# Kernel optimization log

Hardware: AMD Instinct MI355X
Metric: run time of the kernel (lower is better)

Reference implementation:

```python
import jax, jax.numpy as jnp
import numpy as np

NG = 1024      # graphs
NPG = 128      # nodes per graph (forced by lin1 = Linear(128*hid, 128))
N = NG * NPG   # 131072 nodes
DEG = 16       # avg in-graph degree
E = N * DEG    # 2,097,152 edges
IN, H = 4, 64


def setup_inputs() -> dict:
    key = jax.random.key(0)
    ks = jax.random.split(key, 24)
    x = jax.random.normal(ks[0], (N, IN), jnp.float32)
    # edges constrained within each 128-node graph
    src = jax.random.randint(ks[1], (E,), 0, NPG)
    dst = jax.random.randint(ks[2], (E,), 0, NPG)
    off = jnp.repeat(jnp.arange(NG, dtype=jnp.int32) * NPG, NPG * DEG)
    edge_index = jnp.stack([src.astype(jnp.int32) + off, dst.astype(jnp.int32) + off])
    g = lambda k, shp, fan: jax.random.normal(k, shp, jnp.float32) / np.float32(np.sqrt(fan))
    return {
        "x": x, "edge_index": edge_index,
        # GATv2Conv(4->64)
        "Wl": g(ks[3], (IN, H), IN), "bl": jnp.zeros((H,), jnp.float32),
        "Wr": g(ks[4], (IN, H), IN), "br": jnp.zeros((H,), jnp.float32),
        "att_v2": g(ks[5], (H,), H), "b_v2": jnp.zeros((H,), jnp.float32),
        # GATConv #1 (64->64)
        "Wg1": g(ks[6], (H, H), H), "as1": g(ks[7], (H,), H),
        "ad1": g(ks[8], (H,), H), "bg1": jnp.zeros((H,), jnp.float32),
        # GATConv #2 (64->64)
        "Wg2": g(ks[9], (H, H), H), "as2": g(ks[10], (H,), H),
        "ad2": g(ks[11], (H,), H), "bg2": jnp.zeros((H,), jnp.float32),
        # LayerNorm(64)
        "ln_g": jnp.ones((H,), jnp.float32), "ln_b": jnp.zeros((H,), jnp.float32),
        # heads: Linear(128*64 -> 128), Linear(128 -> 1)
        "W1": g(ks[12], (NPG * H, 128), NPG * H), "b1": jnp.zeros((128,), jnp.float32),
        "W2": g(ks[13], (128, 1), 128), "b2": jnp.zeros((1,), jnp.float32),
    }


def _seg_softmax(logits, seg):
    # stable softmax over edges grouped by destination node
    m = jax.ops.segment_max(logits, seg, num_segments=N)
    ex = jnp.exp(logits - m[seg])
    s = jax.ops.segment_sum(ex, seg, num_segments=N)
    return ex / (s[seg] + 1e-16)


def _gatv2(x, src, dst, Wl, bl, Wr, br, att, bias):
    xl = x @ Wl + bl                       # source transform [N,H]
    xr = x @ Wr + br                       # target transform [N,H]
    e = jax.nn.leaky_relu(xl[src] + xr[dst], 0.2) @ att   # [E]
    a = _seg_softmax(e, dst)
    out = jax.ops.segment_sum(a[:, None] * xl[src], dst, num_segments=N)
    return out + bias


def _gat(x, src, dst, W, a_src, a_dst, bias):
    # GATConv default: add self-loops
    loop = jnp.arange(N, dtype=src.dtype)
    s2 = jnp.concatenate([src, loop]); d2 = jnp.concatenate([dst, loop])
    xw = x @ W                             # [N,H]
    al_s = xw @ a_src; al_d = xw @ a_dst   # per-node attention halves [N]
    e = jax.nn.leaky_relu(al_s[s2] + al_d[d2], 0.2)
    a = _seg_softmax(e, d2)
    out = jax.ops.segment_sum(a[:, None] * xw[s2], d2, num_segments=N)
    return out + bias


def _layernorm(x, g, b, eps=1e-5):
    mu = jnp.mean(x, -1, keepdims=True)
    var = jnp.mean(jnp.square(x - mu), -1, keepdims=True)
    return (x - mu) * jax.lax.rsqrt(var + eps) * g + b


def reference(x, edge_index, Wl, bl, Wr, br, att_v2, b_v2,
              Wg1, as1, ad1, bg1, Wg2, as2, ad2, bg2,
              ln_g, ln_b, W1, b1, W2, b2):
    src, dst = edge_index[0], edge_index[1]
    h = jax.nn.leaky_relu(_gatv2(x, src, dst, Wl, bl, Wr, br, att_v2, b_v2), 0.01)
    h = _layernorm(h, ln_g, ln_b)
    h = jax.nn.relu(_gat(h, src, dst, Wg1, as1, ad1, bg1))
    h = jax.nn.relu(_gat(h, src, dst, Wg2, as2, ad2, bg2))
    # linearize: batch is sorted with exactly NPG nodes per graph -> reshape
    h = h.reshape(NG, NPG * H)
    h = jax.nn.leaky_relu(h @ W1 + b1, 0.01)
    return jax.nn.sigmoid(h @ W2 + b2)     # [NG, 1]
```

## Files before the change

kernel.cpp:

```cpp
#include <hip/hip_runtime.h>
#include <hip/hip_bf16.h>

#define NGRAPH 1024
#define NPG 128
#define NTOT (NGRAPH*NPG)
#define EPG 2048
#define ETOT (NTOT*16)
#define HD 64

typedef unsigned int uint;
typedef unsigned short ushort_t;
typedef __attribute__((ext_vector_type(8))) short s8v;
typedef __attribute__((ext_vector_type(4))) float f32x4;

#define MFMA16 __builtin_amdgcn_mfma_f32_16x16x32_bf16

__device__ __forceinline__ float lrelu(float x, float s){ return fmaxf(x, x*s); }
__device__ __forceinline__ float b2lo(uint u){ return __uint_as_float(u << 16); }
__device__ __forceinline__ float b2hi(uint u){ return __uint_as_float(u & 0xFFFF0000u); }
__device__ __forceinline__ uint pkbf(float a, float b){
  union { __hip_bfloat162 h; uint u; } t;
  t.h = __hip_bfloat162{__float2bfloat16(a), __float2bfloat16(b)};
  return t.u;
}
__device__ __forceinline__ ushort_t bfb(float v){
  __hip_bfloat16 h = __float2bfloat16(v);
  union { __hip_bfloat16 h; ushort_t u; } t; t.h = h; return t.u;
}
union U4S8 { uint4 u; s8v s; };
__device__ __forceinline__ s8v bcs8(uint4 u){ U4S8 t; t.u = u; return t.s; }
__device__ __forceinline__ s8v pk8(uint4 x, uint4 y){
  U4S8 t;
  t.u.x = pkbf(__uint_as_float(x.x), __uint_as_float(x.y));
  t.u.y = pkbf(__uint_as_float(x.z), __uint_as_float(x.w));
  t.u.z = pkbf(__uint_as_float(y.x), __uint_as_float(y.y));
  t.u.w = pkbf(__uint_as_float(y.z), __uint_as_float(y.w));
  return t.s;
}

#define DPP_ADD(v, ctrl) ((v) + __int_as_float(__builtin_amdgcn_update_dpp(0, __float_as_int(v), (ctrl), 0xF, 0xF, false)))

__device__ __forceinline__ int oswz(int r, int p){ return (r<<5) | ((((p>>2) ^ (r & 7))<<2) | (p & 3)); }
__device__ __forceinline__ int obase(int r, int oc){ return (r<<5) | (((oc) ^ (r & 7))<<2); }
__device__ __forceinline__ int t64(int r, int p){ return (r<<6) | ((((p>>2) ^ (r & 15))<<2) | (p & 3)); }
__device__ __forceinline__ int t64b(int r, int q){ return (r<<6) | (((q ^ (r & 15))<<2)); }
__device__ __forceinline__ int fP(int r, int k){ return (r<<7) | (((((k>>2) ^ r) & 31)<<2) | (k & 3)); }
__device__ __forceinline__ int fPb(int r, int q){ return (r<<7) | ((((q ^ r) & 31))<<2); }

#define O_A   0
#define O_B   4096
#define O_P   8192
#define O_EV  10240
#define O_ED  11264
#define O_SOF 12288
#define O_SPO 12417
#define O_NMV 12545
#define O_SSE 12673
#define O_ALS 12801
#define O_ALD 12929
#define O_WAS 13060
#define O_WAD 13124
#define SM_SZ 13188

__global__ __launch_bounds__(256) void gnn_fused(
    const float* __restrict__ x, const int* __restrict__ ei,
    const float* __restrict__ Wl, const float* __restrict__ bl,
    const float* __restrict__ Wr, const float* __restrict__ br,
    const float* __restrict__ att, const float* __restrict__ bv2,
    const float* __restrict__ Wg1, const float* __restrict__ as1,
    const float* __restrict__ ad1, const float* __restrict__ bg1,
    const float* __restrict__ Wg2, const float* __restrict__ as2,
    const float* __restrict__ ad2, const float* __restrict__ bg2,
    const float* __restrict__ lng, const float* __restrict__ lnb,
    uint* __restrict__ hout)
{
  __shared__ uint SM[SM_SZ];
  uint*      sXl  = SM + O_A;
  uint*      sXr  = SM + O_B;
  float*     Pf   = (float*)(SM + O_P);
  _Float16*  evh  = (_Float16*)(SM + O_EV);
  ushort_t*  edsd = (ushort_t*)(SM + O_ED);
  int*       soff = (int*)(SM + O_SOF);
  int*       spos = (int*)(SM + O_SPO);
  float*     nmv  = (float*)(SM + O_NMV);
  float*     sse  = (float*)(SM + O_SSE);
  float*     als  = (float*)(SM + O_ALS);
  float*     ald  = (float*)(SM + O_ALD);
  float*     was  = (float*)(SM + O_WAS);
  float*     wad  = (float*)(SM + O_WAD);
  ushort_t*  sH16 = (ushort_t*)(SM + O_A);
  ushort_t*  sT16 = (ushort_t*)(SM + O_B);
  ushort_t*  wg16 = (ushort_t*)(SM + O_P);

  const int g    = blockIdx.x;
  const int tid  = threadIdx.x;
  const int lane = tid & 63;
  const int wv   = tid >> 6;
  const int lw   = lane & 15;
  const int lq   = lane >> 4;
  const int oc   = lane & 7;
  const int ebase = g * EPG;

  if (tid < NPG) spos[tid] = 0;
  __syncthreads();
  for (int e = tid; e < EPG; e += 256)
    atomicAdd(&spos[ei[ETOT + ebase + e] - g*NPG], 1);
  __syncthreads();
  if (wv == 0) {
    int c0 = spos[lane], c1 = spos[lane + 64];
    #pragma unroll
    for (int o = 1; o < 64; o <<= 1) { int t = __shfl_up(c0, o); if (lane >= o) c0 += t; }
    #pragma unroll
    for (int o = 1; o < 64; o <<= 1) { int t = __shfl_up(c1, o); if (lane >= o) c1 += t; }
    int tot0 = __shfl(c0, 63);
    soff[lane + 1]  = c0;
    soff[lane + 65] = c1 + tot0;
    if (lane == 0) soff[0] = 0;
  }
  __syncthreads();
  if (tid < NPG) spos[tid] = soff[tid];
  __syncthreads();
  for (int e = tid; e < EPG; e += 256) {
    int s = ei[ebase + e] - g*NPG;
    int d = ei[ETOT + ebase + e] - g*NPG;
    int p = atomicAdd(&spos[d], 1);
    edsd[p] = (ushort_t)(s | (d << 8));
  }

  {
    const int pl = lane & 31, hb = lane >> 5;
    const float2 wl0 = *(const float2*)&Wl[0*64 + 2*pl];
    const float2 wl1 = *(const float2*)&Wl[1*64 + 2*pl];
    const float2 wl2 = *(const float2*)&Wl[2*64 + 2*pl];
    const float2 wl3 = *(const float2*)&Wl[3*64 + 2*pl];
    const float2 wr0 = *(const float2*)&Wr[0*64 + 2*pl];
    const float2 wr1 = *(const float2*)&Wr[1*64 + 2*pl];
    const float2 wr2 = *(const float2*)&Wr[2*64 + 2*pl];
    const float2 wr3 = *(const float2*)&Wr[3*64 + 2*pl];
    const float2 blp = *(const float2*)&bl[2*pl];
    const float2 brp = *(const float2*)&br[2*pl];
    const float4* x4 = (const float4*)x + (size_t)g * NPG;
    __syncthreads();
    for (int st = 0; st < 16; st++) {
      int i = st*8 + wv*2 + hb;
      float4 xi = x4[i];
      float l0 = blp.x + xi.x*wl0.x + xi.y*wl1.x + xi.z*wl2.x + xi.w*wl3.x;
      float l1 = blp.y + xi.x*wl0.y + xi.y*wl1.y + xi.z*wl2.y + xi.w*wl3.y;
      float r0 = brp.x + xi.x*wr0.x + xi.y*wr1.x + xi.z*wr2.x + xi.w*wr3.x;
      float r1 = brp.y + xi.x*wr0.y + xi.y*wr1.y + xi.z*wr2.y + xi.w*wr3.y;
      sXl[oswz(i, pl)] = pkbf(l0, l1);
      sXr[oswz(i, pl)] = pkbf(r0, r1);
    }
  }
  __syncthreads();

  {
    const int grp = lane >> 3;
    float4 atA = *(const float4*)&att[oc*8];
    float4 atB = *(const float4*)&att[oc*8 + 4];
    int base = wv * 512;
    for (int stp = 0; stp < 64; stp++) {
      int e  = base + stp*8 + grp;
      int sd = edsd[e];
      int s  = sd & 127, d = sd >> 8;
      uint4 ql = *(uint4*)&sXl[obase(s, oc)];
      uint4 qr = *(uint4*)&sXr[obase(d, oc)];
      float acc, v;
      v = b2lo(ql.x)+b2lo(qr.x); acc  = lrelu(v,0.2f)*atA.x;
      v = b2hi(ql.x)+b2hi(qr.x); acc += lrelu(v,0.2f)*atA.y;
      v = b2lo(ql.y)+b2lo(qr.y); acc += lrelu(v,0.2f)*atA.z;
      v = b2hi(ql.y)+b2hi(qr.y); acc += lrelu(v,0.2f)*atA.w;
      v = b2lo(ql.z)+b2lo(qr.z); acc += lrelu(v,0.2f)*atB.x;
      v = b2hi(ql.z)+b2hi(qr.z); acc += lrelu(v,0.2f)*atB.y;
      v = b2lo(ql.w)+b2lo(qr.w); acc += lrelu(v,0.2f)*atB.z;
      v = b2hi(ql.w)+b2hi(qr.w); acc += lrelu(v,0.2f)*atB.w;
      acc = DPP_ADD(acc, 0x111); acc = DPP_ADD(acc, 0x112); acc = DPP_ADD(acc, 0x114);
      if ((lane & 7) == 7) Pf[e] = acc;
    }
  }
  __syncthreads();

  {
    const int g16 = tid >> 4, sl = tid & 15;
    for (int it = 0; it < 8; it++) {
      int d = it*16 + g16;
      int p0 = soff[d], p1 = soff[d+1];
      float m = -1e30f;
      for (int p = p0 + sl; p < p1; p += 16) m = fmaxf(m, Pf[p]);
      #pragma unroll
      for (int o = 1; o < 16; o <<= 1) m = fmaxf(m, __shfl_xor(m, o));
      float ssum = 0.f;
      for (int p = p0 + sl; p < p1; p += 16) {
        float ex = __expf(Pf[p] - m); ssum += ex; evh[p] = (_Float16)ex;
      }
      #pragma unroll
      for (int o = 1; o < 16; o <<= 1) ssum += __shfl_xor(ssum, o);
      if (sl == 0) nmv[d] = 1.f / (ssum + 1e-16f);
    }
    ushort_t* xl16 = (ushort_t*)(SM + O_A);
    int j = tid & 63, spb = tid >> 6;
    for (int i = 0; i < 16; i++) {
      int sp = spb*16 + i;
      float v0 = __uint_as_float((uint)xl16[oswz(2*sp,   j>>1)*2 + (j&1)] << 16);
      float v1 = __uint_as_float((uint)xl16[oswz(2*sp+1, j>>1)*2 + (j&1)] << 16);
      sXr[t64(j, sp)] = pkbf(v0, v1);
    }
  }
  __syncthreads();

  {
    int n0 = 16*wv;
    float bja = bv2[n0 + lw];
    int jc0 = n0 + lw;
    for (int q = 0; q < 8; q++) {
      #pragma unroll
      for (int i = 0; i < 2; i++) { uint4 z = {0,0,0,0}; *(uint4*)&SM[O_P + (tid + i*256)*4] = z; }
      __syncthreads();
      int p0 = soff[q*16], p1 = soff[q*16 + 16];
      for (int p = p0 + tid; p < p1; p += 256) {
        int sd = edsd[p]; int s = sd & 127, d = sd >> 8;
        atomicAdd(&Pf[fP(d - q*16, s)], (float)evh[p] * nmv[d]);
      }
      __syncthreads();
      f32x4 c0 = {0.f,0.f,0.f,0.f};
      #pragma unroll
      for (int ks = 0; ks < 4; ks++) {
        int kk = ks*32 + lq*8;
        uint4 f0 = *(uint4*)&Pf[fPb(lw, kk>>2)];
        uint4 f1 = *(uint4*)&Pf[fPb(lw, (kk>>2)+1)];
        s8v a = pk8(f0, f1);
        s8v b0 = bcs8(*(uint4*)&SM[O_B + t64b(n0 + lw, kk>>3)]);
        c0 = MFMA16(a, b0, c0, 0, 0, 0);
      }
      int rg0 = q*16 + lq*4;
      #pragma unroll
      for (int rg = 0; rg < 4; rg++) {
        float v0 = lrelu(c0[rg] + bja, 0.01f);
        sH16[oswz(rg0+rg, jc0>>1)*2 + (jc0&1)] = bfb(v0);
      }
      __syncthreads();
    }
  }

  {
    int pl = lane & 31, hb = lane >> 5;
    float2 gv = *(const float2*)&lng[2*pl];
    float2 bv = *(const float2*)&lnb[2*pl];
    for (int it = 0; it < 16; it++) {
      int d = it*8 + wv*2 + hb;
      uint w = SM[O_A + oswz(d, pl)];
      float v0 = b2lo(w), v1 = b2hi(w);
      float s1 = v0 + v1, s2 = v0*v0 + v1*v1;
      #pragma unroll
      for (int o = 1; o < 32; o <<= 1) { s1 += __shfl_xor(s1, o); s2 += __shfl_xor(s2, o); }
      float mu  = s1 * 0.015625f;
      float var = s2 * 0.015625f - mu*mu;
      float rs  = rsqrtf(var + 1e-5f);
      v0 = (v0 - mu)*rs*gv.x + bv.x;
      v1 = (v1 - mu)*rs*gv.y + bv.y;
      SM[O_A + oswz(d, pl)] = pkbf(v0, v1);
    }
  }
  __syncthreads();

  for (int layer = 0; layer < 2; layer++) {
    const float* Wg  = layer ? Wg2 : Wg1;
    const float* avs = layer ? as2 : as1;
    const float* avd = layer ? ad2 : ad1;
    const float* bg  = layer ? bg2 : bg1;

    if (tid < 128) {
      const float* av = (tid < 64) ? avs : avd;
      float* dst = (tid < 64) ? was : wad;
      int k = tid & 63;
      float acc = 0.f;
      #pragma unroll
      for (int jj = 0; jj < 16; jj++) {
        float4 w = *(const float4*)&Wg[k*64 + jj*4];
        float4 a = *(const float4*)&av[jj*4];
        acc += w.x*a.x + w.y*a.y + w.z*a.z + w.w*a.w;
      }
      dst[k] = acc;
    } else {
      int t2 = tid - 128;
      #pragma unroll
      for (int i = 0; i < 8; i++) {
        int idx = t2 + i*128;
        int k = idx >> 4, j4 = (idx & 15)*4;
        float4 w = *(const float4*)&Wg[k*64 + j4];
        wg16[oswz(j4+0, k>>1)*2 + (k&1)] = bfb(w.x);
        wg16[oswz(j4+1, k>>1)*2 + (k&1)] = bfb(w.y);
        wg16[oswz(j4+2, k>>1)*2 + (k&1)] = bfb(w.z);
        wg16[oswz(j4+3, k>>1)*2 + (k&1)] = bfb(w.w);
      }
    }
    __syncthreads();

    {
      int row = 16*wv + lw;
      s8v a0 = bcs8(*(uint4*)&SM[O_P + obase(row, lq)]);
      s8v a1 = bcs8(*(uint4*)&SM[O_P + obase(row, 4+lq)]);
      #pragma unroll
      for (int nt = 0; nt < 8; nt++) {
        int d = nt*16 + lw;
        s8v b0 = bcs8(*(uint4*)&SM[O_A + obase(d, lq)]);
        s8v b1 = bcs8(*(uint4*)&SM[O_A + obase(d, 4+lq)]);
        f32x4 c = {0.f,0.f,0.f,0.f};
        c = MFMA16(a0, b0, c, 0, 0, 0);
        c = MFMA16(a1, b1, c, 0, 0, 0);
        int j0 = 16*wv + lq*4;
        #pragma unroll
        for (int rg = 0; rg < 4; rg++)
          sT16[t64(j0+rg, d>>1)*2 + (d&1)] = bfb(c[rg]);
      }
    }
    __syncthreads();

    {
      float4 ws0 = *(float4*)&was[oc*8], ws1 = *(float4*)&was[oc*8 + 4];
      float4 wd0 = *(float4*)&wad[oc*8], wd1 = *(float4*)&wad[oc*8 + 4];
      for (int ps = 0; ps < 4; ps++) {
        int n = ps*32 + (tid >> 3);
        uint4 qv = *(uint4*)&SM[O_A + obase(n, oc)];
        float f0=b2lo(qv.x), f1=b2hi(qv.x), f2=b2lo(qv.y), f3=b2hi(qv.y);
        float f4=b2lo(qv.z), f5=b2hi(qv.z), f6=b2lo(qv.w), f7=b2hi(qv.w);
        float sa = f0*ws0.x+f1*ws0.y+f2*ws0.z+f3*ws0.w+f4*ws1.x+f5*ws1.y+f6*ws1.z+f7*ws1.w;
        float sd = f0*wd0.x+f1*wd0.y+f2*wd0.z+f3*wd0.w+f4*wd1.x+f5*wd1.y+f6*wd1.z+f7*wd1.w;
        sa = DPP_ADD(sa, 0x111); sa = DPP_ADD(sa, 0x112); sa = DPP_ADD(sa, 0x114);
        sd = DPP_ADD(sd, 0x111); sd = DPP_ADD(sd, 0x112); sd = DPP_ADD(sd, 0x114);
        if ((lane & 7) == 7) { als[n] = sa; ald[n] = sd; }
      }
    }
    __syncthreads();

    {
      const int g16 = tid >> 4, sl = tid & 15;
      for (int it = 0; it < 8; it++) {
        int d = it*16 + g16;
        int p0 = soff[d], p1 = soff[d+1];
        float adv = ald[d];
        float se = lrelu(als[d] + adv, 0.2f);
        float m = se;
        for (int p = p0 + sl; p < p1; p += 16)
          m = fmaxf(m, lrelu(als[edsd[p] & 127] + adv, 0.2f));
        #pragma unroll
        for (int o = 1; o < 16; o <<= 1) m = fmaxf(m, __shfl_xor(m, o));
        float ex0 = __expf(se - m);
        float ssum = 0.f;
        for (int p = p0 + sl; p < p1; p += 16) {
          float ex = __expf(lrelu(als[edsd[p] & 127] + adv, 0.2f) - m);
          ssum += ex; evh[p] = (_Float16)ex;
        }
        #pragma unroll
        for (int o = 1; o < 16; o <<= 1) ssum += __shfl_xor(ssum, o);
        if (sl == 0) { nmv[d] = 1.f / (ssum + ex0 + 1e-16f); sse[d] = ex0; }
      }
    }
    __syncthreads();

    {
      int n0 = 16*wv;
      float bja = bg[n0 + lw];
      int jc0 = n0 + lw;
      for (int q = 0; q < 8; q++) {
        #pragma unroll
        for (int i = 0; i < 2; i++) { uint4 z = {0,0,0,0}; *(uint4*)&SM[O_P + (tid + i*256)*4] = z; }
        __syncthreads();
        int p0 = soff[q*16], p1 = soff[q*16 + 16];
        for (int p = p0 + tid; p < p1; p += 256) {
          int sd = edsd[p]; int s = sd & 127, d = sd >> 8;
          atomicAdd(&Pf[fP(d - q*16, s)], (float)evh[p] * nmv[d]);
        }
        if (tid < 16) { int d = q*16 + tid; atomicAdd(&Pf[fP(tid, d)], sse[d] * nmv[d]); }
        __syncthreads();
        f32x4 c0 = {0.f,0.f,0.f,0.f};
        #pragma unroll
        for (int ks = 0; ks < 4; ks++) {
          int kk = ks*32 + lq*8;
          uint4 f0 = *(uint4*)&Pf[fPb(lw, kk>>2)];
          uint4 f1 = *(uint4*)&Pf[fPb(lw, (kk>>2)+1)];
          s8v a = pk8(f0, f1);
          s8v b0 = bcs8(*(uint4*)&SM[O_B + t64b(n0 + lw, kk>>3)]);
          c0 = MFMA16(a, b0, c0, 0, 0, 0);
        }
        int rg0 = q*16 + lq*4;
        #pragma unroll
        for (int rg = 0; rg < 4; rg++) {
          float v0 = fmaxf(c0[rg] + bja, 0.f);
          sH16[oswz(rg0+rg, jc0>>1)*2 + (jc0&1)] = bfb(v0);
        }
        __syncthreads();
      }
    }
  }

  {
    uint* hg = hout + (size_t)g * 4096;
    #pragma unroll
    for (int i = 0; i < 16; i++) {
      int idx = tid + i*256;
      hg[idx] = SM[O_A + oswz(idx >> 5, idx & 31)];
    }
  }
}

__global__ __launch_bounds__(256) void w1_transpose(const float* __restrict__ W1,
                                                    uint* __restrict__ w1t)
{
  __shared__ float sw[64*130];
  const int tid = threadIdx.x;
  const int k0 = blockIdx.x * 64;
  #pragma unroll
  for (int i = 0; i < 8; i++) {
    int idx = tid + i*256;
    int r = idx >> 5, c4 = (idx & 31)*4;
    *(float4*)&sw[r*130 + c4] = *(const float4*)&W1[(size_t)(k0+r)*128 + c4];
  }
  __syncthreads();
  #pragma unroll
  for (int i = 0; i < 16; i++) {
    int idx = tid + i*256;
    int c = idx >> 5, kp = idx & 31;
    w1t[(size_t)c*4096 + (k0>>1) + kp] = pkbf(sw[(2*kp)*130 + c], sw[(2*kp+1)*130 + c]);
  }
}

__global__ __launch_bounds__(256) void head_gemm(
    const uint* __restrict__ hbuf, const uint* __restrict__ w1t,
    float* __restrict__ partial)
{
  __shared__ uint sAh[2048];
  __shared__ uint sBh[4096];
  const int tid = threadIdx.x, lane = tid & 63, wv = tid >> 6;
  const int lw = lane & 15, lq = lane >> 4;
  const int g0 = blockIdx.x * 64;
  const int ks = blockIdx.y;
  f32x4 acc[8];
  #pragma unroll
  for (int i = 0; i < 8; i++) acc[i] = f32x4{0.f,0.f,0.f,0.f};

  for (int ch = 0; ch < 8; ch++) {
    int pb = ks*256 + ch*32;
    #pragma unroll
    for (int i = 0; i < 2; i++) {
      int idx = tid + i*256; int r = idx >> 3, q4 = idx & 7;
      uint4 v = *(const uint4*)&hbuf[(size_t)(g0+r)*4096 + pb + q4*4];
      *(uint4*)&sAh[(r<<5) | ((q4 ^ (r & 7))<<2)] = v;
    }
    #pragma unroll
    for (int i = 0; i < 4; i++) {
      int idx = tid + i*256; int r = idx >> 3, q4 = idx & 7;
      uint4 v = *(const uint4*)&w1t[(size_t)r*4096 + pb + q4*4];
      *(uint4*)&sBh[(r<<5) | ((q4 ^ (r & 7))<<2)] = v;
    }
    __syncthreads();
    int ra = 16*wv + lw;
    s8v a0 = bcs8(*(uint4*)&sAh[obase(ra, lq)]);
    s8v a1 = bcs8(*(uint4*)&sAh[obase(ra, 4+lq)]);
    #pragma unroll
    for (int nt = 0; nt < 8; nt++) {
      int c = nt*16 + lw;
      s8v b0 = bcs8(*(uint4*)&sBh[obase(c, lq)]);
      s8v b1 = bcs8(*(uint4*)&sBh[obase(c, 4+lq)]);
      acc[nt] = MFMA16(a0, b0, acc[nt], 0, 0, 0);
      acc[nt] = MFMA16(a1, b1, acc[nt], 0, 0, 0);
    }
    __syncthreads();
  }
  float* pp = partial + (size_t)ks*131072;
  #pragma unroll
  for (int nt = 0; nt < 8; nt++) {
    int c = nt*16 + lw;
    int r0 = g0 + 16*wv + lq*4;
    #pragma unroll
    for (int rg = 0; rg < 4; rg++)
      pp[(size_t)(r0+rg)*128 + c] = acc[nt][rg];
  }
}

__global__ __launch_bounds__(64) void head_out(
    const float* __restrict__ partial, const float* __restrict__ b1,
    const float* __restrict__ W2, const float* __restrict__ b2,
    float* __restrict__ out)
{
  const int g = blockIdx.x;
  const int l = threadIdx.x;
  float v0 = b1[l], v1 = b1[64 + l];
  #pragma unroll
  for (int s = 0; s < 16; s++) {
    v0 += partial[(size_t)s*131072 + g*128 + l];
    v1 += partial[(size_t)s*131072 + g*128 + 64 + l];
  }
  float sum = lrelu(v0, 0.01f)*W2[l] + lrelu(v1, 0.01f)*W2[64 + l];
  #pragma unroll
  for (int m = 32; m > 0; m >>= 1) sum += __shfl_xor(sum, m);
  if (l == 0) out[g] = 1.f / (1.f + __expf(-(sum + b2[0])));
}

extern "C" void kernel_launch(void* const* d_in, const int* in_sizes, int n_in,
                              void* d_out, int out_size, void* d_ws, size_t ws_size,
                              hipStream_t stream) {
  const float* x   = (const float*)d_in[0];
  const int*   ei  = (const int*)  d_in[1];
  const float* Wl  = (const float*)d_in[2];
  const float* bl_ = (const float*)d_in[3];
  const float* Wr  = (const float*)d_in[4];
  const float* br_ = (const float*)d_in[5];
  const float* att = (const float*)d_in[6];
  const float* bv2 = (const float*)d_in[7];
  const float* Wg1 = (const float*)d_in[8];
  const float* as1 = (const float*)d_in[9];
  const float* ad1 = (const float*)d_in[10];
  const float* bg1 = (const float*)d_in[11];
  const float* Wg2 = (const float*)d_in[12];
  const float* as2 = (const float*)d_in[13];
  const float* ad2 = (const float*)d_in[14];
  const float* bg2 = (const float*)d_in[15];
  const float* lng = (const float*)d_in[16];
  const float* lnb = (const float*)d_in[17];
  const float* W1  = (const float*)d_in[18];
  const float* b1  = (const float*)d_in[19];
  const float* W2  = (const float*)d_in[20];
  const float* b2  = (const float*)d_in[21];
  float* out = (float*)d_out;

  uint*  hbuf    = (uint*)d_ws;
  float* partial = (float*)((char*)d_ws + (size_t)16*1024*1024);
  uint*  w1t     = (uint*)((char*)d_ws + (size_t)24*1024*1024);

  w1_transpose<<<128, 256, 0, stream>>>(W1, w1t);
  gnn_fused<<<NGRAPH, 256, 0, stream>>>(x, ei, Wl, bl_, Wr, br_, att, bv2,
      Wg1, as1, ad1, bg1, Wg2, as2, ad2, bg2, lng, lnb, hbuf);
  head_gemm<<<dim3(16, 16), 256, 0, stream>>>(hbuf, w1t, partial);
  head_out<<<NGRAPH, 64, 0, stream>>>(partial, b1, W2, b2, out);
}
```

Measured before the change: 305.6 us.

## Replace dense-P MFMA aggregation with per-node sparse gather FMA and shrink LDS

The attention aggregation no longer materialises a dense 16x128 P matrix through LDS atomics and multiplies it with MFMA. Each thread pair now owns one destination node and directly accumulates weighted bf16 source features over its CSR edge list in registers, with LayerNorm fused into the GATv2 epilogue. The GATv2 right transform is computed per destination in registers instead of being stored in LDS, and the x@W matmul moves to a fuller MFMA tile. LDS per block drops from about 52KB to about 38KB, and launch bounds now request 4 blocks per SM. The cost is a large register footprint from 32-float accumulators, serial per-node edge loops with load imbalance, and uncoalesced LDS gathers.

```diff
diff --git a/kernel.cpp b/kernel.cpp
--- a/kernel.cpp
+++ b/kernel.cpp
@@ -29,40 +29,50 @@
 }
 union U4S8 { uint4 u; s8v s; };
 __device__ __forceinline__ s8v bcs8(uint4 u){ U4S8 t; t.u = u; return t.s; }
-__device__ __forceinline__ s8v pk8(uint4 x, uint4 y){
-  U4S8 t;
-  t.u.x = pkbf(__uint_as_float(x.x), __uint_as_float(x.y));
-  t.u.y = pkbf(__uint_as_float(x.z), __uint_as_float(x.w));
-  t.u.z = pkbf(__uint_as_float(y.x), __uint_as_float(y.y));
-  t.u.w = pkbf(__uint_as_float(y.z), __uint_as_float(y.w));
-  return t.s;
-}
 
 #define DPP_ADD(v, ctrl) ((v) + __int_as_float(__builtin_amdgcn_update_dpp(0, __float_as_int(v), (ctrl), 0xF, 0xF, false)))
 
 __device__ __forceinline__ int oswz(int r, int p){ return (r<<5) | ((((p>>2) ^ (r & 7))<<2) | (p & 3)); }
 __device__ __forceinline__ int obase(int r, int oc){ return (r<<5) | (((oc) ^ (r & 7))<<2); }
-__device__ __forceinline__ int t64(int r, int p){ return (r<<6) | ((((p>>2) ^ (r & 15))<<2) | (p & 3)); }
-__device__ __forceinline__ int t64b(int r, int q){ return (r<<6) | (((q ^ (r & 15))<<2)); }
-__device__ __forceinline__ int fP(int r, int k){ return (r<<7) | (((((k>>2) ^ r) & 31)<<2) | (k & 3)); }
-__device__ __forceinline__ int fPb(int r, int q){ return (r<<7) | ((((q ^ r) & 31))<<2); }
-
-#define O_A   0
-#define O_B   4096
-#define O_P   8192
-#define O_EV  10240
-#define O_ED  11264
-#define O_SOF 12288
-#define O_SPO 12417
-#define O_NMV 12545
-#define O_SSE 12673
-#define O_ALS 12801
-#define O_ALD 12929
-#define O_WAS 13060
-#define O_WAD 13124
-#define SM_SZ 13188
-
-__global__ __launch_bounds__(256) void gnn_fused(
+
+#define O_F   0
+#define O_W   4096
+#define O_EV  6144
+#define O_ED  7168
+#define O_X   8192
+#define O_SOF 8704
+#define O_SPO 8833
+#define O_NMV 8961
+#define O_SSE 9089
+#define O_ALS 9217
+#define O_ALD 9345
+#define O_WAS 9476
+#define O_WAD 9540
+#define SM_SZ 9604
+
+#define GFMA(s, a) { \
+    uint4 q0 = *(uint4*)&SM[O_F + obase((s), 4*hf+0)]; \
+    uint4 q1 = *(uint4*)&SM[O_F + obase((s), 4*hf+1)]; \
+    uint4 q2 = *(uint4*)&SM[O_F + obase((s), 4*hf+2)]; \
+    uint4 q3 = *(uint4*)&SM[O_F + obase((s), 4*hf+3)]; \
+    acc[0]  += (a)*b2lo(q0.x); acc[1]  += (a)*b2hi(q0.x); \
+    acc[2]  += (a)*b2lo(q0.y); acc[3]  += (a)*b2hi(q0.y); \
+    acc[4]  += (a)*b2lo(q0.z); acc[5]  += (a)*b2hi(q0.z); \
+    acc[6]  += (a)*b2lo(q0.w); acc[7]  += (a)*b2hi(q0.w); \
+    acc[8]  += (a)*b2lo(q1.x); acc[9]  += (a)*b2hi(q1.x); \
+    acc[10] += (a)*b2lo(q1.y); acc[11] += (a)*b2hi(q1.y); \
+    acc[12] += (a)*b2lo(q1.z); acc[13] += (a)*b2hi(q1.z); \
+    acc[14] += (a)*b2lo(q1.w); acc[15] += (a)*b2hi(q1.w); \
+    acc[16] += (a)*b2lo(q2.x); acc[17] += (a)*b2hi(q2.x); \
+    acc[18] += (a)*b2lo(q2.y); acc[19] += (a)*b2hi(q2.y); \
+    acc[20] += (a)*b2lo(q2.z); acc[21] += (a)*b2hi(q2.z); \
+    acc[22] += (a)*b2lo(q2.w); acc[23] += (a)*b2hi(q2.w); \
+    acc[24] += (a)*b2lo(q3.x); acc[25] += (a)*b2hi(q3.x); \
+    acc[26] += (a)*b2lo(q3.y); acc[27] += (a)*b2hi(q3.y); \
+    acc[28] += (a)*b2lo(q3.z); acc[29] += (a)*b2hi(q3.z); \
+    acc[30] += (a)*b2lo(q3.w); acc[31] += (a)*b2hi(q3.w); }
+
+__global__ __launch_bounds__(256, 4) void gnn_fused(
     const float* __restrict__ x, const int* __restrict__ ei,
     const float* __restrict__ Wl, const float* __restrict__ bl,
     const float* __restrict__ Wr, const float* __restrict__ br,
@@ -75,9 +85,7 @@
     uint* __restrict__ hout)
 {
   __shared__ uint SM[SM_SZ];
-  uint*      sXl  = SM + O_A;
-  uint*      sXr  = SM + O_B;
-  float*     Pf   = (float*)(SM + O_P);
+  uint*      sXl  = SM + O_F;
   _Float16*  evh  = (_Float16*)(SM + O_EV);
   ushort_t*  edsd = (ushort_t*)(SM + O_ED);
   int*       soff = (int*)(SM + O_SOF);
@@ -88,9 +96,9 @@
   float*     ald  = (float*)(SM + O_ALD);
   float*     was  = (float*)(SM + O_WAS);
   float*     wad  = (float*)(SM + O_WAD);
-  ushort_t*  sH16 = (ushort_t*)(SM + O_A);
-  ushort_t*  sT16 = (ushort_t*)(SM + O_B);
-  ushort_t*  wg16 = (ushort_t*)(SM + O_P);
+  ushort_t*  sH16 = (ushort_t*)(SM + O_F);
+  ushort_t*  wg16 = (ushort_t*)(SM + O_W);
+  float*     lgf  = (float*)(SM + O_W);
 
   const int g    = blockIdx.x;
   const int tid  = threadIdx.x;
@@ -128,54 +136,62 @@
   }
 
   {
+    const float4* x4g = (const float4*)x + (size_t)g * NPG;
+    float4* sx4w = (float4*)(SM + O_X);
+    if (tid < NPG) sx4w[tid] = x4g[tid];
     const int pl = lane & 31, hb = lane >> 5;
     const float2 wl0 = *(const float2*)&Wl[0*64 + 2*pl];
     const float2 wl1 = *(const float2*)&Wl[1*64 + 2*pl];
     const float2 wl2 = *(const float2*)&Wl[2*64 + 2*pl];
     const float2 wl3 = *(const float2*)&Wl[3*64 + 2*pl];
-    const float2 wr0 = *(const float2*)&Wr[0*64 + 2*pl];
-    const float2 wr1 = *(const float2*)&Wr[1*64 + 2*pl];
-    const float2 wr2 = *(const float2*)&Wr[2*64 + 2*pl];
-    const float2 wr3 = *(const float2*)&Wr[3*64 + 2*pl];
     const float2 blp = *(const float2*)&bl[2*pl];
-    const float2 brp = *(const float2*)&br[2*pl];
-    const float4* x4 = (const float4*)x + (size_t)g * NPG;
-    __syncthreads();
     for (int st = 0; st < 16; st++) {
       int i = st*8 + wv*2 + hb;
-      float4 xi = x4[i];
+      float4 xi = x4g[i];
       float l0 = blp.x + xi.x*wl0.x + xi.y*wl1.x + xi.z*wl2.x + xi.w*wl3.x;
       float l1 = blp.y + xi.x*wl0.y + xi.y*wl1.y + xi.z*wl2.y + xi.w*wl3.y;
-      float r0 = brp.x + xi.x*wr0.x + xi.y*wr1.x + xi.z*wr2.x + xi.w*wr3.x;
-      float r1 = brp.y + xi.x*wr0.y + xi.y*wr1.y + xi.z*wr2.y + xi.w*wr3.y;
       sXl[oswz(i, pl)] = pkbf(l0, l1);
-      sXr[oswz(i, pl)] = pkbf(r0, r1);
     }
   }
   __syncthreads();
 
   {
-    const int grp = lane >> 3;
-    float4 atA = *(const float4*)&att[oc*8];
-    float4 atB = *(const float4*)&att[oc*8 + 4];
-    int base = wv * 512;
-    for (int stp = 0; stp < 64; stp++) {
-      int e  = base + stp*8 + grp;
-      int sd = edsd[e];
-      int s  = sd & 127, d = sd >> 8;
-      uint4 ql = *(uint4*)&sXl[obase(s, oc)];
-      uint4 qr = *(uint4*)&sXr[obase(d, oc)];
-      float acc, v;
-      v = b2lo(ql.x)+b2lo(qr.x); acc  = lrelu(v,0.2f)*atA.x;
-      v = b2hi(ql.x)+b2hi(qr.x); acc += lrelu(v,0.2f)*atA.y;
-      v = b2lo(ql.y)+b2lo(qr.y); acc += lrelu(v,0.2f)*atA.z;
-      v = b2hi(ql.y)+b2hi(qr.y); acc += lrelu(v,0.2f)*atA.w;
-      v = b2lo(ql.z)+b2lo(qr.z); acc += lrelu(v,0.2f)*atB.x;
-      v = b2hi(ql.z)+b2hi(qr.z); acc += lrelu(v,0.2f)*atB.y;
-      v = b2lo(ql.w)+b2lo(qr.w); acc += lrelu(v,0.2f)*atB.z;
-      v = b2hi(ql.w)+b2hi(qr.w); acc += lrelu(v,0.2f)*atB.w;
-      acc = DPP_ADD(acc, 0x111); acc = DPP_ADD(acc, 0x112); acc = DPP_ADD(acc, 0x114);
-      if ((lane & 7) == 7) Pf[e] = acc;
+    const float4* sx4 = (const float4*)(SM + O_X);
+    const int grp8 = lane >> 3;
+    float4 w0a = *(const float4*)&Wr[0*64 + oc*8], w0b = *(const float4*)&Wr[0*64 + oc*8 + 4];
+    float4 w1a = *(const float4*)&Wr[1*64 + oc*8], w1b = *(const float4*)&Wr[1*64 + oc*8 + 4];
+    float4 w2a = *(const float4*)&Wr[2*64 + oc*8], w2b = *(const float4*)&Wr[2*64 + oc*8 + 4];
+    float4 w3a = *(const float4*)&Wr[3*64 + oc*8], w3b = *(const float4*)&Wr[3*64 + oc*8 + 4];
+    float4 bra = *(const float4*)&br[oc*8],  brb = *(const float4*)&br[oc*8 + 4];
+    float4 atA = *(const float4*)&att[oc*8], atB = *(const float4*)&att[oc*8 + 4];
+    for (int it = 0; it < 4; it++) {
+      int d = it*32 + wv*8 + grp8;
+      float4 xd = sx4[d];
+      float4 xra, xrb;
+      xra.x = bra.x + xd.x*w0a.x + xd.y*w1a.x + xd.z*w2a.x + xd.w*w3a.x;
+      xra.y = bra.y + xd.x*w0a.y + xd.y*w1a.y + xd.z*w2a.y + xd.w*w3a.y;
+      xra.z = bra.z + xd.x*w0a.z + xd.y*w1a.z + xd.z*w2a.z + xd.w*w3a.z;
+      xra.w = bra.w + xd.x*w0a.w + xd.y*w1a.w + xd.z*w2a.w + xd.w*w3a.w;
+      xrb.x = brb.x + xd.x*w0b.x + xd.y*w1b.x + xd.z*w2b.x + xd.w*w3b.x;
+      xrb.y = brb.y + xd.x*w0b.y + xd.y*w1b.y + xd.z*w2b.y + xd.w*w3b.y;
+      xrb.z = brb.z + xd.x*w0b.z + xd.y*w1b.z + xd.z*w2b.z + xd.w*w3b.z;
+      xrb.w = brb.w + xd.x*w0b.w + xd.y*w1b.w + xd.z*w2b.w + xd.w*w3b.w;
+      int p0 = soff[d], p1 = soff[d+1];
+      for (int p = p0; p < p1; p++) {
+        int s = edsd[p] & 127;
+        uint4 ql = *(uint4*)&SM[O_F + obase(s, oc)];
+        float e, v;
+        v = b2lo(ql.x)+xra.x; e  = lrelu(v,0.2f)*atA.x;
+        v = b2hi(ql.x)+xra.y; e += lrelu(v,0.2f)*atA.y;
+        v = b2lo(ql.y)+xra.z; e += lrelu(v,0.2f)*atA.z;
+        v = b2hi(ql.y)+xra.w; e += lrelu(v,0.2f)*atA.w;
+        v = b2lo(ql.z)+xrb.x; e += lrelu(v,0.2f)*atB.x;
+        v = b2hi(ql.z)+xrb.y; e += lrelu(v,0.2f)*atB.y;
+        v = b2lo(ql.w)+xrb.z; e += lrelu(v,0.2f)*atB.z;
+        v = b2hi(ql.w)+xrb.w; e += lrelu(v,0.2f)*atB.w;
+        e = DPP_ADD(e, 0x111); e = DPP_ADD(e, 0x112); e = DPP_ADD(e, 0x114);
+        if (oc == 7) lgf[p] = e;
+      }
     }
   }
   __syncthreads();
@@ -186,80 +202,61 @@
       int d = it*16 + g16;
       int p0 = soff[d], p1 = soff[d+1];
       float m = -1e30f;
-      for (int p = p0 + sl; p < p1; p += 16) m = fmaxf(m, Pf[p]);
+      for (int p = p0 + sl; p < p1; p += 16) m = fmaxf(m, lgf[p]);
       #pragma unroll
       for (int o = 1; o < 16; o <<= 1) m = fmaxf(m, __shfl_xor(m, o));
       float ssum = 0.f;
       for (int p = p0 + sl; p < p1; p += 16) {
-        float ex = __expf(Pf[p] - m); ssum += ex; evh[p] = (_Float16)ex;
+        float ex = __expf(lgf[p] - m); ssum += ex; evh[p] = (_Float16)ex;
       }
       #pragma unroll
       for (int o = 1; o < 16; o <<= 1) ssum += __shfl_xor(ssum, o);
       if (sl == 0) nmv[d] = 1.f / (ssum + 1e-16f);
     }
-    ushort_t* xl16 = (ushort_t*)(SM + O_A);
-    int j = tid & 63, spb = tid >> 6;
-    for (int i = 0; i < 16; i++) {
-      int sp = spb*16 + i;
-      float v0 = __uint_as_float((uint)xl16[oswz(2*sp,   j>>1)*2 + (j&1)] << 16);
-      float v1 = __uint_as_float((uint)xl16[oswz(2*sp+1, j>>1)*2 + (j&1)] << 16);
-      sXr[t64(j, sp)] = pkbf(v0, v1);
-    }
   }
   __syncthreads();
 
   {
-    int n0 = 16*wv;
-    float bja = bv2[n0 + lw];
-    int jc0 = n0 + lw;
-    for (int q = 0; q < 8; q++) {
-      #pragma unroll
-      for (int i = 0; i < 2; i++) { uint4 z = {0,0,0,0}; *(uint4*)&SM[O_P + (tid + i*256)*4] = z; }
-      __syncthreads();
-      int p0 = soff[q*16], p1 = soff[q*16 + 16];
-      for (int p = p0 + tid; p < p1; p += 256) {
-        int sd = edsd[p]; int s = sd & 127, d = sd >> 8;
-        atomicAdd(&Pf[fP(d - q*16, s)], (float)evh[p] * nmv[d]);
-      }
-      __syncthreads();
-      f32x4 c0 = {0.f,0.f,0.f,0.f};
-      #pragma unroll
-      for (int ks = 0; ks < 4; ks++) {
-        int kk = ks*32 + lq*8;
-        uint4 f0 = *(uint4*)&Pf[fPb(lw, kk>>2)];
-        uint4 f1 = *(uint4*)&Pf[fPb(lw, (kk>>2)+1)];
-        s8v a = pk8(f0, f1);
-        s8v b0 = bcs8(*(uint4*)&SM[O_B + t64b(n0 + lw, kk>>3)]);
-        c0 = MFMA16(a, b0, c0, 0, 0, 0);
-      }
-      int rg0 = q*16 + lq*4;
-      #pragma unroll
-      for (int rg = 0; rg < 4; rg++) {
-        float v0 = lrelu(c0[rg] + bja, 0.01f);
-        sH16[oswz(rg0+rg, jc0>>1)*2 + (jc0&1)] = bfb(v0);
-      }
-      __syncthreads();
-    }
-  }
-
-  {
-    int pl = lane & 31, hb = lane >> 5;
-    float2 gv = *(const float2*)&lng[2*pl];
-    float2 bv = *(const float2*)&lnb[2*pl];
-    for (int it = 0; it < 16; it++) {
-      int d = it*8 + wv*2 + hb;
-      uint w = SM[O_A + oswz(d, pl)];
-      float v0 = b2lo(w), v1 = b2hi(w);
-      float s1 = v0 + v1, s2 = v0*v0 + v1*v1;
-      #pragma unroll
-      for (int o = 1; o < 32; o <<= 1) { s1 += __shfl_xor(s1, o); s2 += __shfl_xor(s2, o); }
-      float mu  = s1 * 0.015625f;
-      float var = s2 * 0.015625f - mu*mu;
-      float rs  = rsqrtf(var + 1e-5f);
-      v0 = (v0 - mu)*rs*gv.x + bv.x;
-      v1 = (v1 - mu)*rs*gv.y + bv.y;
-      SM[O_A + oswz(d, pl)] = pkbf(v0, v1);
-    }
+    const int d = tid >> 1, hf = tid & 1;
+    int p0 = soff[d], p1 = soff[d+1];
+    float nmv_d = nmv[d];
+    float acc[32];
+    #pragma unroll
+    for (int i = 0; i < 32; i++) acc[i] = 0.f;
+    for (int p = p0; p < p1; p++) {
+      int s = edsd[p] & 127;
+      float a = nmv_d * (float)evh[p];
+      GFMA(s, a)
+    }
+    float s1 = 0.f, s2 = 0.f;
+    #pragma unroll
+    for (int j = 0; j < 8; j++) {
+      float4 bq = *(const float4*)&bv2[hf*32 + j*4];
+      float v0 = lrelu(acc[j*4+0] + bq.x, 0.01f);
+      float v1 = lrelu(acc[j*4+1] + bq.y, 0.01f);
+      float v2 = lrelu(acc[j*4+2] + bq.z, 0.01f);
+      float v3 = lrelu(acc[j*4+3] + bq.w, 0.01f);
+      acc[j*4+0]=v0; acc[j*4+1]=v1; acc[j*4+2]=v2; acc[j*4+3]=v3;
+      s1 += v0+v1+v2+v3;
+      s2 += v0*v0+v1*v1+v2*v2+v3*v3;
+    }
+    s1 += __shfl_xor(s1, 1); s2 += __shfl_xor(s2, 1);
+    float mu  = s1 * 0.015625f;
+    float var = s2 * 0.015625f - mu*mu;
+    float rs  = rsqrtf(var + 1e-5f);
+    #pragma unroll
+    for (int j = 0; j < 8; j++) {
+      float4 gq = *(const float4*)&lng[hf*32 + j*4];
+      float4 bq = *(const float4*)&lnb[hf*32 + j*4];
+      acc[j*4+0] = (acc[j*4+0]-mu)*rs*gq.x + bq.x;
+      acc[j*4+1] = (acc[j*4+1]-mu)*rs*gq.y + bq.y;
+      acc[j*4+2] = (acc[j*4+2]-mu)*rs*gq.z + bq.z;
+      acc[j*4+3] = (acc[j*4+3]-mu)*rs*gq.w + bq.w;
+    }
+    __syncthreads();
+    #pragma unroll
+    for (int pp = 0; pp < 16; pp++)
+      sXl[oswz(d, hf*16 + pp)] = pkbf(acc[2*pp], acc[2*pp+1]);
   }
   __syncthreads();
 
@@ -297,31 +294,11 @@
     __syncthreads();
 
     {
-      int row = 16*wv + lw;
-      s8v a0 = bcs8(*(uint4*)&SM[O_P + obase(row, lq)]);
-      s8v a1 = bcs8(*(uint4*)&SM[O_P + obase(row, 4+lq)]);
-      #pragma unroll
-      for (int nt = 0; nt < 8; nt++) {
-        int d = nt*16 + lw;
-        s8v b0 = bcs8(*(uint4*)&SM[O_A + obase(d, lq)]);
-        s8v b1 = bcs8(*(uint4*)&SM[O_A + obase(d, 4+lq)]);
-        f32x4 c = {0.f,0.f,0.f,0.f};
-        c = MFMA16(a0, b0, c, 0, 0, 0);
-        c = MFMA16(a1, b1, c, 0, 0, 0);
-        int j0 = 16*wv + lq*4;
-        #pragma unroll
-        for (int rg = 0; rg < 4; rg++)
-          sT16[t64(j0+rg, d>>1)*2 + (d&1)] = bfb(c[rg]);
-      }
-    }
-    __syncthreads();
-
-    {
       float4 ws0 = *(float4*)&was[oc*8], ws1 = *(float4*)&was[oc*8 + 4];
       float4 wd0 = *(float4*)&wad[oc*8], wd1 = *(float4*)&wad[oc*8 + 4];
       for (int ps = 0; ps < 4; ps++) {
         int n = ps*32 + (tid >> 3);
-        uint4 qv = *(uint4*)&SM[O_A + obase(n, oc)];
+        uint4 qv = *(uint4*)&SM[O_F + obase(n, oc)];
         float f0=b2lo(qv.x), f1=b2hi(qv.x), f2=b2lo(qv.y), f3=b2hi(qv.y);
         float f4=b2lo(qv.z), f5=b2hi(qv.z), f6=b2lo(qv.w), f7=b2hi(qv.w);
         float sa = f0*ws0.x+f1*ws0.y+f2*ws0.z+f3*ws0.w+f4*ws1.x+f5*ws1.y+f6*ws1.z+f7*ws1.w;
@@ -333,6 +310,37 @@
     }
     __syncthreads();
 
+    {
+      const int r0 = 32*wv;
+      uint4 a00 = *(uint4*)&SM[O_F + obase(r0+lw,    lq  )];
+      uint4 a01 = *(uint4*)&SM[O_F + obase(r0+lw,    4+lq)];
+      uint4 a10 = *(uint4*)&SM[O_F + obase(r0+16+lw, lq  )];
+      uint4 a11 = *(uint4*)&SM[O_F + obase(r0+16+lw, 4+lq)];
+      uint4 bfr[4][2];
+      #pragma unroll
+      for (int nt = 0; nt < 4; nt++) {
+        bfr[nt][0] = *(uint4*)&SM[O_W + obase(nt*16+lw, lq  )];
+        bfr[nt][1] = *(uint4*)&SM[O_W + obase(nt*16+lw, 4+lq)];
+      }
+      f32x4 c0[4], c1[4];
+      #pragma unroll
+      for (int nt = 0; nt < 4; nt++) {
+        f32x4 z = {0.f,0.f,0.f,0.f};
+        c0[nt] = MFMA16(bcs8(a00), bcs8(bfr[nt][0]), z, 0, 0, 0);
+        c0[nt] = MFMA16(bcs8(a01), bcs8(bfr[nt][1]), c0[nt], 0, 0, 0);
+        c1[nt] = MFMA16(bcs8(a10), bcs8(bfr[nt][0]), z, 0, 0, 0);
+        c1[nt] = MFMA16(bcs8(a11), bcs8(bfr[nt][1]), c1[nt], 0, 0, 0);
+      }
+      #pragma unroll
+      for (int nt = 0; nt < 4; nt++) {
+        int col = nt*16 + lw;
+        #pragma unroll
+        for (int rg = 0; rg < 4; rg++) {
+          sH16[oswz(r0 + lq*4 + rg,      col>>1)*2 + (col&1)] = bfb(c0[nt][rg]);
+          sH16[oswz(r0 + 16 + lq*4 + rg, col>>1)*2 + (col&1)] = bfb(c1[nt][rg]);
+        }
+      }
+    }
     {
       const int g16 = tid >> 4, sl = tid & 15;
       for (int it = 0; it < 8; it++) {
@@ -359,39 +367,35 @@
     __syncthreads();
 
     {
-      int n0 = 16*wv;
-      float bja = bg[n0 + lw];
-      int jc0 = n0 + lw;
-      for (int q = 0; q < 8; q++) {
-        #pragma unroll
-        for (int i = 0; i < 2; i++) { uint4 z = {0,0,0,0}; *(uint4*)&SM[O_P + (tid + i*256)*4] = z; }
-        __syncthreads();
-        int p0 = soff[q*16], p1 = soff[q*16 + 16];
-        for (int p = p0 + tid; p < p1; p += 256) {
-          int sd = edsd[p]; int s = sd & 127, d = sd >> 8;
-          atomicAdd(&Pf[fP(d - q*16, s)], (float)evh[p] * nmv[d]);
-        }
-        if (tid < 16) { int d = q*16 + tid; atomicAdd(&Pf[fP(tid, d)], sse[d] * nmv[d]); }
-        __syncthreads();
-        f32x4 c0 = {0.f,0.f,0.f,0.f};
-        #pragma unroll
-        for (int ks = 0; ks < 4; ks++) {
-          int kk = ks*32 + lq*8;
-          uint4 f0 = *(uint4*)&Pf[fPb(lw, kk>>2)];
-          uint4 f1 = *(uint4*)&Pf[fPb(lw, (kk>>2)+1)];
-          s8v a = pk8(f0, f1);
-          s8v b0 = bcs8(*(uint4*)&SM[O_B + t64b(n0 + lw, kk>>3)]);
-          c0 = MFMA16(a, b0, c0, 0, 0, 0);
-        }
-        int rg0 = q*16 + lq*4;
-        #pragma unroll
-        for (int rg = 0; rg < 4; rg++) {
-          float v0 = fmaxf(c0[rg] + bja, 0.f);
-          sH16[oswz(rg0+rg, jc0>>1)*2 + (jc0&1)] = bfb(v0);
-        }
-        __syncthreads();
-      }
-    }
+      const int d = tid >> 1, hf = tid & 1;
+      int p0 = soff[d], p1 = soff[d+1];
+      float nmv_d = nmv[d];
+      float acc[32];
+      #pragma unroll
+      for (int i = 0; i < 32; i++) acc[i] = 0.f;
+      {
+        float a0 = sse[d] * nmv_d;
+        GFMA(d, a0)
+      }
+      for (int p = p0; p < p1; p++) {
+        int s = edsd[p] & 127;
+        float a = nmv_d * (float)evh[p];
+        GFMA(s, a)
+      }
+      #pragma unroll
+      for (int j = 0; j < 8; j++) {
+        float4 bq = *(const float4*)&bg[hf*32 + j*4];
+        acc[j*4+0] = fmaxf(acc[j*4+0] + bq.x, 0.f);
+        acc[j*4+1] = fmaxf(acc[j*4+1] + bq.y, 0.f);
+        acc[j*4+2] = fmaxf(acc[j*4+2] + bq.z, 0.f);
+        acc[j*4+3] = fmaxf(acc[j*4+3] + bq.w, 0.f);
+      }
+      __syncthreads();
+      #pragma unroll
+      for (int pp = 0; pp < 16; pp++)
+        sXl[oswz(d, hf*16 + pp)] = pkbf(acc[2*pp], acc[2*pp+1]);
+    }
+    __syncthreads();
   }
 
   {
@@ -399,7 +403,7 @@
     #pragma unroll
     for (int i = 0; i < 16; i++) {
       int idx = tid + i*256;
-      hg[idx] = SM[O_A + oswz(idx >> 5, idx & 31)];
+      hg[idx] = SM[O_F + oswz(idx >> 5, idx & 31)];
     }
   }
 }
```

Measured after the change: 259.9 us. -15.0%, faster.
